# Performance work log

Measured on AMD Instinct MI355X. Metric: run time of the kernel, lower is better.

## Reference

```python
import jax, jax.numpy as jnp
import numpy as np

B, L, D, H = 4, 2048, 1024, 64  # batch, seq, d_model, head_size

def setup_inputs() -> dict:
    key = jax.random.key(0)
    k1, k2 = jax.random.split(key)
    x = jax.random.normal(k1, (B, L, D), dtype=jnp.float32)
    # nn.Linear(d_model, head_size, bias=False) weight: [head_size, d_model]
    Wq = jax.random.normal(k2, (H, D), dtype=jnp.float32) * (1.0 / np.sqrt(D))
    return {"x": x, "Wq": Wq}

def reference(x, Wq):
    # Faithful to source bug: q, k, v ALL use the query projection.
    q = jnp.einsum('bld,hd->blh', x, Wq)
    k = q
    v = q
    d_k = x.shape[-1]  # source uses d_model, not head_size
    scores = jnp.einsum('blh,bmh->blm', q, k) / jnp.sqrt(jnp.float32(d_k))
    Lq = x.shape[1]
    causal = jnp.tril(jnp.ones((Lq, Lq), dtype=bool))
    scores = jnp.where(causal, scores, -jnp.inf)
    attn = jax.nn.softmax(scores, axis=-1)
    # dropout in eval mode -> identity
    return jnp.einsum('blm,bmh->blh', attn, v)
```

## Files before the change

### kernel.cpp

```cpp
#include <hip/hip_runtime.h>
#include <cmath>

#define Bb 4
#define Ll 2048
#define Dd 1024
#define Hh 64

#define QSCL 0.21233050f

typedef float f32x4 __attribute__((ext_vector_type(4)));
typedef short s16x8 __attribute__((ext_vector_type(8)));

__device__ __forceinline__ unsigned int cvtpk(float a, float b) {
    unsigned int r;
    asm("v_cvt_pk_bf16_f32 %0, %1, %2" : "=v"(r) : "v"(a), "v"(b));
    return r;
}

__device__ __forceinline__ void gload16(const void* g, void* l) {
    __builtin_amdgcn_global_load_lds((__attribute__((address_space(1))) const void*)g,
                                     (__attribute__((address_space(3))) void*)l, 16, 0, 0);
}

__global__ __launch_bounds__(256) void wq_cvt(const float* __restrict__ Wq,
                                              unsigned short* __restrict__ wqb) {
    const int idx = blockIdx.x * 256 + threadIdx.x;
    const int c   = idx >> 11;
    const int kc  = (idx >> 6) & 31;
    const int hsw = idx & 63;
    const int h   = hsw ^ kc;
    const float* src = Wq + (size_t)h * Dd + c * 256 + kc * 8;
    float4 a = *(const float4*)src;
    float4 b = *(const float4*)(src + 4);
    uint4 p; p.x = cvtpk(a.x, a.y); p.y = cvtpk(a.z, a.w);
    p.z = cvtpk(b.x, b.y); p.w = cvtpk(b.z, b.w);
    *(uint4*)(wqb + (size_t)idx * 8) = p;
}

__global__ __launch_bounds__(256, 2) void proj_mfma(const float* __restrict__ x,
                                                    const unsigned short* __restrict__ wqb,
                                                    unsigned short* __restrict__ q,
                                                    unsigned short* __restrict__ qT) {
    __shared__ uint4 xs4[2][32 * 16];
    __shared__ uint4 ws4[2][32 * 64];
    const int t = threadIdx.x;
    const int lane = t & 63, w = t >> 6;
    const int m15 = lane & 15, q_ = lane >> 4;
    const int row0 = blockIdx.x * 16;
    const int kc = t & 31, rr = t >> 5;
    const float* xsrc0 = x + (size_t)(row0 + rr) * Dd + kc * 8;
    const float* xsrc1 = x + (size_t)(row0 + rr + 8) * Dd + kc * 8;

    float4 xa0 = *(const float4*)xsrc0, xb0 = *(const float4*)(xsrc0 + 4);
    float4 xa1 = *(const float4*)xsrc1, xb1 = *(const float4*)(xsrc1 + 4);
#pragma unroll
    for (int j = 0; j < 8; ++j) {
        int off = t + j * 256;
        gload16(wqb + (size_t)off * 8, (char*)ws4[0] + off * 16);
    }
    {
        uint4 p0; p0.x = cvtpk(xa0.x, xa0.y); p0.y = cvtpk(xa0.z, xa0.w);
        p0.z = cvtpk(xb0.x, xb0.y); p0.w = cvtpk(xb0.z, xb0.w);
        xs4[0][kc * 16 + (rr ^ (kc & 15))] = p0;
        uint4 p1; p1.x = cvtpk(xa1.x, xa1.y); p1.y = cvtpk(xa1.z, xa1.w);
        p1.z = cvtpk(xb1.x, xb1.y); p1.w = cvtpk(xb1.z, xb1.w);
        xs4[0][kc * 16 + ((rr + 8) ^ (kc & 15))] = p1;
    }
    xa0 = *(const float4*)(xsrc0 + 256); xb0 = *(const float4*)(xsrc0 + 260);
    xa1 = *(const float4*)(xsrc1 + 256); xb1 = *(const float4*)(xsrc1 + 260);

    f32x4 acc = {0.f, 0.f, 0.f, 0.f};
    for (int c = 0; c < 4; ++c) {
        const int p = c & 1;
        __syncthreads();
        if (c + 1 < 4) {
#pragma unroll
            for (int j = 0; j < 8; ++j) {
                int off = t + j * 256;
                gload16(wqb + (size_t)(c + 1) * 16384 + (size_t)off * 8,
                        (char*)ws4[p ^ 1] + off * 16);
            }
            uint4 p0; p0.x = cvtpk(xa0.x, xa0.y); p0.y = cvtpk(xa0.z, xa0.w);
            p0.z = cvtpk(xb0.x, xb0.y); p0.w = cvtpk(xb0.z, xb0.w);
            xs4[p ^ 1][kc * 16 + (rr ^ (kc & 15))] = p0;
            uint4 p1; p1.x = cvtpk(xa1.x, xa1.y); p1.y = cvtpk(xa1.z, xa1.w);
            p1.z = cvtpk(xb1.x, xb1.y); p1.w = cvtpk(xb1.z, xb1.w);
            xs4[p ^ 1][kc * 16 + ((rr + 8) ^ (kc & 15))] = p1;
            if (c + 2 < 4) {
                xa0 = *(const float4*)(xsrc0 + (c + 2) * 256);
                xb0 = *(const float4*)(xsrc0 + (c + 2) * 256 + 4);
                xa1 = *(const float4*)(xsrc1 + (c + 2) * 256);
                xb1 = *(const float4*)(xsrc1 + (c + 2) * 256 + 4);
            }
        }
#pragma unroll
        for (int ks = 0; ks < 8; ++ks) {
            int kk = ks * 4 + q_;
            s16x8 A = *(const s16x8*)&xs4[p][kk * 16 + (m15 ^ (kk & 15))];
            s16x8 B = *(const s16x8*)&ws4[p][kk * 64 + ((w * 16 + m15) ^ kk)];
            acc = __builtin_amdgcn_mfma_f32_16x16x32_bf16(A, B, acc, 0, 0, 0);
        }
    }
    const int h = w * 16 + m15;
    const int hc = h >> 3, he = h & 7;
    const size_t T = (size_t)(row0 >> 6);
    const int rbase = (row0 & 63) + q_ * 4;
    unsigned int a01 = cvtpk(acc[0] * QSCL, acc[1] * QSCL);
    unsigned int a23 = cvtpk(acc[2] * QSCL, acc[3] * QSCL);
    unsigned short u[4] = { (unsigned short)(a01 & 0xFFFF), (unsigned short)(a01 >> 16),
                            (unsigned short)(a23 & 0xFFFF), (unsigned short)(a23 >> 16) };
#pragma unroll
    for (int i = 0; i < 4; ++i) {
        int rsw = (rbase + i) ^ hc;
        q[((T * 8 + hc) * 64 + rsw) * 8 + he] = u[i];
    }
    unsigned int t01 = cvtpk(acc[0], acc[1]);
    unsigned int t23 = cvtpk(acc[2], acc[3]);
    const int b = row0 >> 11;
    const int m0 = (row0 & 2047) + q_ * 4;
    const int vt = m0 >> 6, cc = (m0 >> 3) & 7, me = m0 & 7;
    const int hsw = h ^ cc;
    ushort4 pk4;
    pk4.x = (unsigned short)(t01 & 0xFFFF); pk4.y = (unsigned short)(t01 >> 16);
    pk4.z = (unsigned short)(t23 & 0xFFFF); pk4.w = (unsigned short)(t23 >> 16);
    *(ushort4*)&qT[(((size_t)(b * 32 + vt) * 8 + cc) * 64 + hsw) * 8 + me] = pk4;
}

__global__ __launch_bounds__(256, 3) void flash_mfma(const unsigned short* __restrict__ qg,
                                                     const unsigned short* __restrict__ qTg,
                                                     float* __restrict__ PO,
                                                     float* __restrict__ ML) {
    const int qt = blockIdx.x;
    const int s  = blockIdx.y;
    const int b  = blockIdx.z;
    if (s > (qt >> 2)) return;
    __shared__ uint4 Qs4[512];
    __shared__ uint4 Ks4[2][512];
    __shared__ uint4 Vt4[2][512];
    __shared__ __align__(16) unsigned short Pb[4 * 16 * 72];
    const int t = threadIdx.x, lane = t & 63, w = t >> 6;
    const int m15 = lane & 15, q_ = lane >> 4;
    const int n_it = min(4, qt - 4 * s + 1);
    const int tb = b * 32;
    const unsigned short* qsrc = qg + (size_t)(tb + qt) * 4096;

#pragma unroll
    for (int j = 0; j < 2; ++j) {
        int off = t + j * 256;
        gload16(qsrc + (size_t)off * 8, (char*)Qs4 + off * 16);
        gload16(qg  + (size_t)(tb + s * 4) * 4096 + (size_t)off * 8, (char*)Ks4[0] + off * 16);
        gload16(qTg + (size_t)(tb + s * 4) * 4096 + (size_t)off * 8, (char*)Vt4[0] + off * 16);
    }
    f32x4 Oacc[4];
#pragma unroll
    for (int i = 0; i < 4; ++i) Oacc[i] = (f32x4){0.f, 0.f, 0.f, 0.f};
    float mr = -INFINITY, lr = 0.f;
    unsigned short* Pr = Pb + (w * 16 + m15) * 72;

    for (int it = 0; it < n_it; ++it) {
        const int pp = it & 1;
        __syncthreads();
        if (it + 1 < n_it) {
            const unsigned short* k2 = qg  + (size_t)(tb + s * 4 + it + 1) * 4096;
            const unsigned short* v2 = qTg + (size_t)(tb + s * 4 + it + 1) * 4096;
#pragma unroll
            for (int j = 0; j < 2; ++j) {
                int off = t + j * 256;
                gload16(k2 + (size_t)off * 8, (char*)Ks4[pp ^ 1] + off * 16);
                gload16(v2 + (size_t)off * 8, (char*)Vt4[pp ^ 1] + off * 16);
            }
        }
        f32x4 sc[4];
#pragma unroll
        for (int ct = 0; ct < 4; ++ct) sc[ct] = (f32x4){0.f, 0.f, 0.f, 0.f};
        __builtin_amdgcn_s_setprio(1);
#pragma unroll
        for (int ks = 0; ks < 2; ++ks) {
            const int hc = ks * 4 + q_;
            s16x8 Bq = *(const s16x8*)&Qs4[hc * 64 + ((w * 16 + m15) ^ hc)];
#pragma unroll
            for (int ct = 0; ct < 4; ++ct) {
                s16x8 Ak = *(const s16x8*)&Ks4[pp][hc * 64 + ((ct * 16 + m15) ^ hc)];
                sc[ct] = __builtin_amdgcn_mfma_f32_16x16x32_bf16(Ak, Bq, sc[ct], 0, 0, 0);
            }
        }
        __builtin_amdgcn_s_setprio(0);

        const bool diag = (4 * s + it) == qt;
        float v[16];
        if (diag) {
            const int rel = w * 16 + m15 - q_ * 4;
#pragma unroll
            for (int ct = 0; ct < 4; ++ct)
#pragma unroll
                for (int r = 0; r < 4; ++r)
                    v[ct * 4 + r] = (ct * 16 + r > rel) ? -INFINITY : sc[ct][r];
        } else {
#pragma unroll
            for (int ct = 0; ct < 4; ++ct)
#pragma unroll
                for (int r = 0; r < 4; ++r)
                    v[ct * 4 + r] = sc[ct][r];
        }
        float x01 = fmaxf(v[0], v[1]),  x23 = fmaxf(v[2], v[3]);
        float x45 = fmaxf(v[4], v[5]),  x67 = fmaxf(v[6], v[7]);
        float x89 = fmaxf(v[8], v[9]),  xab = fmaxf(v[10], v[11]);
        float xcd = fmaxf(v[12], v[13]), xef = fmaxf(v[14], v[15]);
        float vmax = fmaxf(fmaxf(fmaxf(x01, x23), fmaxf(x45, x67)),
                           fmaxf(fmaxf(x89, xab), fmaxf(xcd, xef)));
        vmax = fmaxf(vmax, __shfl_xor(vmax, 16, 64));
        vmax = fmaxf(vmax, __shfl_xor(vmax, 32, 64));
        const float mnew = fmaxf(mr, vmax);
        const float alpha = exp2f(mr - mnew);
#pragma unroll
        for (int i = 0; i < 16; ++i) v[i] = exp2f(v[i] - mnew);
        float s01 = (v[0] + v[1]) + (v[2] + v[3]);
        float s23 = (v[4] + v[5]) + (v[6] + v[7]);
        float s45 = (v[8] + v[9]) + (v[10] + v[11]);
        float s67 = (v[12] + v[13]) + (v[14] + v[15]);
        float psum = (s01 + s23) + (s45 + s67);
        psum += __shfl_xor(psum, 16, 64);
        psum += __shfl_xor(psum, 32, 64);
        lr = lr * alpha + psum;
        mr = mnew;
#pragma unroll
        for (int ht = 0; ht < 4; ++ht) Oacc[ht] *= alpha;
#pragma unroll
        for (int ct = 0; ct < 4; ++ct) {
            uint2 pr; pr.x = cvtpk(v[ct * 4 + 0], v[ct * 4 + 1]);
            pr.y = cvtpk(v[ct * 4 + 2], v[ct * 4 + 3]);
            *(uint2*)(Pr + ct * 16 + q_ * 4) = pr;
        }
        __builtin_amdgcn_s_setprio(1);
#pragma unroll
        for (int kc2 = 0; kc2 < 2; ++kc2) {
            const int cc = kc2 * 4 + q_;
            s16x8 Bp = *(const s16x8*)(Pr + kc2 * 32 + q_ * 8);
#pragma unroll
            for (int ht = 0; ht < 4; ++ht) {
                s16x8 Av = *(const s16x8*)&Vt4[pp][cc * 64 + ((ht * 16 + m15) ^ cc)];
                Oacc[ht] = __builtin_amdgcn_mfma_f32_16x16x32_bf16(Av, Bp, Oacc[ht], 0, 0, 0);
            }
        }
        __builtin_amdgcn_s_setprio(0);
    }
    const size_t base = ((size_t)((b * 32 + qt) * 8 + s)) * 4096;
#pragma unroll
    for (int ht = 0; ht < 4; ++ht)
        *(f32x4*)&PO[base + (size_t)(w * 16 + m15) * 64 + ht * 16 + q_ * 4] = Oacc[ht];
    if (q_ == 0) {
        float* mlp = ML + ((size_t)((b * 32 + qt) * 8 + s)) * 128;
        mlp[(w * 16 + m15) * 2 + 0] = mr;
        mlp[(w * 16 + m15) * 2 + 1] = lr;
    }
}

__global__ __launch_bounds__(256) void combine_k(const float* __restrict__ PO,
                                                 const float* __restrict__ ML,
                                                 float* __restrict__ out) {
    const int bq = blockIdx.x;
    const int b = bq >> 5, qt = bq & 31;
    const int ns = (qt >> 2) + 1;
    const int t = threadIdx.x;
    const int r = blockIdx.y * 32 + (t >> 3);
    const int c8 = (t & 7) * 8;
    const float* mlp = ML + (size_t)bq * 8 * 128;
    const float* pob = PO + (size_t)bq * 8 * 4096;
    float M = -INFINITY;
    for (int si = 0; si < ns; ++si) M = fmaxf(M, mlp[si * 128 + r * 2]);
    float L = 0.f;
    f32x4 a0 = {0.f, 0.f, 0.f, 0.f}, a1 = a0;
    for (int si = 0; si < ns; ++si) {
        float ms = mlp[si * 128 + r * 2], ls = mlp[si * 128 + r * 2 + 1];
        float wgt = exp2f(ms - M);
        L += ls * wgt;
        const f32x4* sp = (const f32x4*)(pob + (size_t)si * 4096 + r * 64 + c8);
        a0 += wgt * sp[0];
        a1 += wgt * sp[1];
    }
    float inv = 1.0f / L;
    f32x4* op = (f32x4*)(out + (size_t)(b * Ll + qt * 64 + r) * 64 + c8);
    op[0] = a0 * inv;
    op[1] = a1 * inv;
}

extern "C" void kernel_launch(void* const* d_in, const int* in_sizes, int n_in,
                              void* d_out, int out_size, void* d_ws, size_t ws_size,
                              hipStream_t stream) {
    const float* x  = (const float*)d_in[0];
    const float* Wq = (const float*)d_in[1];
    float* out = (float*)d_out;
    char* ws = (char*)d_ws;
    unsigned short* q   = (unsigned short*)ws;
    unsigned short* qT  = (unsigned short*)(ws + (1 << 20));
    float* PO = (float*)(ws + (2 << 20));
    float* ML = (float*)(ws + (18 << 20));
    unsigned short* wqb = (unsigned short*)(ws + (19 << 20));

    wq_cvt<<<32, 256, 0, stream>>>(Wq, wqb);
    proj_mfma<<<512, 256, 0, stream>>>(x, wqb, q, qT);
    flash_mfma<<<dim3(32, 8, Bb), 256, 0, stream>>>(q, qT, PO, ML);
    combine_k<<<dim3(128, 2), 256, 0, stream>>>(PO, ML, out);
}
```

Baseline: 103.0 us.

## Fuse split-KV combine into flash kernel via last-block atomic counter, compact grid

Removes the separate combine kernel launch: each flash block bumps a per-query-tile atomic counter after writing its partial output, and the last split block to finish performs the log-sum-exp merge and writes the final output. The grid is also compacted from a 3D grid with early-exit blocks into a triangular 1D enumeration of only the valid (query tile, split) pairs. Counters are zeroed inside the projection kernel. This saves one launch and the idle blocks, at the cost of threadfences and a serialized tail combine on the last-arriving block.

```diff
diff --git a/kernel.cpp b/kernel.cpp
--- a/kernel.cpp
+++ b/kernel.cpp
@@ -40,10 +40,12 @@
 __global__ __launch_bounds__(256, 2) void proj_mfma(const float* __restrict__ x,
                                                     const unsigned short* __restrict__ wqb,
                                                     unsigned short* __restrict__ q,
-                                                    unsigned short* __restrict__ qT) {
+                                                    unsigned short* __restrict__ qT,
+                                                    int* __restrict__ cnt) {
     __shared__ uint4 xs4[2][32 * 16];
     __shared__ uint4 ws4[2][32 * 64];
     const int t = threadIdx.x;
+    if (blockIdx.x == 0 && t < 128) cnt[t] = 0;
     const int lane = t & 63, w = t >> 6;
     const int m15 = lane & 15, q_ = lane >> 4;
     const int row0 = blockIdx.x * 16;
@@ -129,15 +131,23 @@
 __global__ __launch_bounds__(256, 3) void flash_mfma(const unsigned short* __restrict__ qg,
                                                      const unsigned short* __restrict__ qTg,
                                                      float* __restrict__ PO,
-                                                     float* __restrict__ ML) {
-    const int qt = blockIdx.x;
-    const int s  = blockIdx.y;
-    const int b  = blockIdx.z;
-    if (s > (qt >> 2)) return;
+                                                     float* __restrict__ ML,
+                                                     int* __restrict__ cnt,
+                                                     float* __restrict__ out) {
+    const int idx = blockIdx.x;
+    const int b   = blockIdx.y;
+    int g = 0;
+    while (2 * (g + 1) * (g + 2) <= idx) ++g;
+    const int local = idx - 2 * g * (g + 1);
+    const int qt = 4 * g + local / (g + 1);
+    const int s  = local % (g + 1);
+    const int ns = g + 1;
+
     __shared__ uint4 Qs4[512];
     __shared__ uint4 Ks4[2][512];
     __shared__ uint4 Vt4[2][512];
     __shared__ __align__(16) unsigned short Pb[4 * 16 * 72];
+    __shared__ int lastFlag;
     const int t = threadIdx.x, lane = t & 63, w = t >> 6;
     const int m15 = lane & 15, q_ = lane >> 4;
     const int n_it = min(4, qt - 4 * s + 1);
@@ -244,44 +254,48 @@
         }
         __builtin_amdgcn_s_setprio(0);
     }
-    const size_t base = ((size_t)((b * 32 + qt) * 8 + s)) * 4096;
+    const int bq = b * 32 + qt;
+    const size_t base = ((size_t)bq * 8 + s) * 4096;
 #pragma unroll
     for (int ht = 0; ht < 4; ++ht)
         *(f32x4*)&PO[base + (size_t)(w * 16 + m15) * 64 + ht * 16 + q_ * 4] = Oacc[ht];
     if (q_ == 0) {
-        float* mlp = ML + ((size_t)((b * 32 + qt) * 8 + s)) * 128;
+        float* mlp = ML + ((size_t)bq * 8 + s) * 128;
         mlp[(w * 16 + m15) * 2 + 0] = mr;
         mlp[(w * 16 + m15) * 2 + 1] = lr;
     }
-}
-
-__global__ __launch_bounds__(256) void combine_k(const float* __restrict__ PO,
-                                                 const float* __restrict__ ML,
-                                                 float* __restrict__ out) {
-    const int bq = blockIdx.x;
-    const int b = bq >> 5, qt = bq & 31;
-    const int ns = (qt >> 2) + 1;
-    const int t = threadIdx.x;
-    const int r = blockIdx.y * 32 + (t >> 3);
-    const int c8 = (t & 7) * 8;
+    __threadfence();
+    __syncthreads();
+    if (t == 0) {
+        int old = atomicAdd(&cnt[bq], 1);
+        lastFlag = (old == ns - 1);
+    }
+    __syncthreads();
+    if (!lastFlag) return;
+    __threadfence();
     const float* mlp = ML + (size_t)bq * 8 * 128;
     const float* pob = PO + (size_t)bq * 8 * 4096;
-    float M = -INFINITY;
-    for (int si = 0; si < ns; ++si) M = fmaxf(M, mlp[si * 128 + r * 2]);
-    float L = 0.f;
-    f32x4 a0 = {0.f, 0.f, 0.f, 0.f}, a1 = a0;
-    for (int si = 0; si < ns; ++si) {
-        float ms = mlp[si * 128 + r * 2], ls = mlp[si * 128 + r * 2 + 1];
-        float wgt = exp2f(ms - M);
-        L += ls * wgt;
-        const f32x4* sp = (const f32x4*)(pob + (size_t)si * 4096 + r * 64 + c8);
-        a0 += wgt * sp[0];
-        a1 += wgt * sp[1];
-    }
-    float inv = 1.0f / L;
-    f32x4* op = (f32x4*)(out + (size_t)(b * Ll + qt * 64 + r) * 64 + c8);
-    op[0] = a0 * inv;
-    op[1] = a1 * inv;
+    const int c8 = (t & 7) * 8;
+#pragma unroll
+    for (int ry = 0; ry < 2; ++ry) {
+        const int r = ry * 32 + (t >> 3);
+        float M = -INFINITY;
+        for (int si = 0; si < ns; ++si) M = fmaxf(M, mlp[si * 128 + r * 2]);
+        float L = 0.f;
+        f32x4 a0 = {0.f, 0.f, 0.f, 0.f}, a1 = a0;
+        for (int si = 0; si < ns; ++si) {
+            float ms = mlp[si * 128 + r * 2], ls = mlp[si * 128 + r * 2 + 1];
+            float wgt = exp2f(ms - M);
+            L += ls * wgt;
+            const f32x4* sp = (const f32x4*)(pob + (size_t)si * 4096 + r * 64 + c8);
+            a0 += wgt * sp[0];
+            a1 += wgt * sp[1];
+        }
+        float inv = 1.0f / L;
+        f32x4* op = (f32x4*)(out + (size_t)(b * Ll + qt * 64 + r) * 64 + c8);
+        op[0] = a0 * inv;
+        op[1] = a1 * inv;
+    }
 }
 
 extern "C" void kernel_launch(void* const* d_in, const int* in_sizes, int n_in,
@@ -296,9 +310,9 @@
     float* PO = (float*)(ws + (2 << 20));
     float* ML = (float*)(ws + (18 << 20));
     unsigned short* wqb = (unsigned short*)(ws + (19 << 20));
+    int* cnt = (int*)(ws + (20 << 20));
 
     wq_cvt<<<32, 256, 0, stream>>>(Wq, wqb);
-    proj_mfma<<<512, 256, 0, stream>>>(x, wqb, q, qT);
-    flash_mfma<<<dim3(32, 8, Bb), 256, 0, stream>>>(q, qT, PO, ML);
-    combine_k<<<dim3(128, 2), 256, 0, stream>>>(PO, ML, out);
-}
+    proj_mfma<<<512, 256, 0, stream>>>(x, wqb, q, qT, cnt);
+    flash_mfma<<<dim3(144, Bb), 256, 0, stream>>>(q, qT, PO, ML, cnt, out);
+}
```

After: 188.9 us. +83.4%, slower.

## Drop split-KV partitioning and normalize attention output directly in flash kernel

Applied to the files above, without the earlier changes.

Each flash block now walks every causal key tile for its query tile instead of at most four. It divides by the running softmax sum and writes the final output itself. This removes the partial-output and max/sum workspace writes and the separate combine kernel launch. The cost is a grid of only 128 blocks with very uneven work: the last query tile runs 32 iterations serially, which can leave many CUs idle and lengthen the critical path.

```diff
diff --git a/kernel.cpp b/kernel.cpp
--- a/kernel.cpp
+++ b/kernel.cpp
@@ -128,19 +128,16 @@
 
 __global__ __launch_bounds__(256, 3) void flash_mfma(const unsigned short* __restrict__ qg,
                                                      const unsigned short* __restrict__ qTg,
-                                                     float* __restrict__ PO,
-                                                     float* __restrict__ ML) {
+                                                     float* __restrict__ out) {
     const int qt = blockIdx.x;
-    const int s  = blockIdx.y;
-    const int b  = blockIdx.z;
-    if (s > (qt >> 2)) return;
+    const int b  = blockIdx.y;
     __shared__ uint4 Qs4[512];
     __shared__ uint4 Ks4[2][512];
     __shared__ uint4 Vt4[2][512];
     __shared__ __align__(16) unsigned short Pb[4 * 16 * 72];
     const int t = threadIdx.x, lane = t & 63, w = t >> 6;
     const int m15 = lane & 15, q_ = lane >> 4;
-    const int n_it = min(4, qt - 4 * s + 1);
+    const int n_it = qt + 1;
     const int tb = b * 32;
     const unsigned short* qsrc = qg + (size_t)(tb + qt) * 4096;
 
@@ -148,8 +145,8 @@
     for (int j = 0; j < 2; ++j) {
         int off = t + j * 256;
         gload16(qsrc + (size_t)off * 8, (char*)Qs4 + off * 16);
-        gload16(qg  + (size_t)(tb + s * 4) * 4096 + (size_t)off * 8, (char*)Ks4[0] + off * 16);
-        gload16(qTg + (size_t)(tb + s * 4) * 4096 + (size_t)off * 8, (char*)Vt4[0] + off * 16);
+        gload16(qg  + (size_t)tb * 4096 + (size_t)off * 8, (char*)Ks4[0] + off * 16);
+        gload16(qTg + (size_t)tb * 4096 + (size_t)off * 8, (char*)Vt4[0] + off * 16);
     }
     f32x4 Oacc[4];
 #pragma unroll
@@ -161,8 +158,8 @@
         const int pp = it & 1;
         __syncthreads();
         if (it + 1 < n_it) {
-            const unsigned short* k2 = qg  + (size_t)(tb + s * 4 + it + 1) * 4096;
-            const unsigned short* v2 = qTg + (size_t)(tb + s * 4 + it + 1) * 4096;
+            const unsigned short* k2 = qg  + (size_t)(tb + it + 1) * 4096;
+            const unsigned short* v2 = qTg + (size_t)(tb + it + 1) * 4096;
 #pragma unroll
             for (int j = 0; j < 2; ++j) {
                 int off = t + j * 256;
@@ -186,7 +183,7 @@
         }
         __builtin_amdgcn_s_setprio(0);
 
-        const bool diag = (4 * s + it) == qt;
+        const bool diag = (it == qt);
         float v[16];
         if (diag) {
             const int rel = w * 16 + m15 - q_ * 4;
@@ -244,44 +241,13 @@
         }
         __builtin_amdgcn_s_setprio(0);
     }
-    const size_t base = ((size_t)((b * 32 + qt) * 8 + s)) * 4096;
-#pragma unroll
-    for (int ht = 0; ht < 4; ++ht)
-        *(f32x4*)&PO[base + (size_t)(w * 16 + m15) * 64 + ht * 16 + q_ * 4] = Oacc[ht];
-    if (q_ == 0) {
-        float* mlp = ML + ((size_t)((b * 32 + qt) * 8 + s)) * 128;
-        mlp[(w * 16 + m15) * 2 + 0] = mr;
-        mlp[(w * 16 + m15) * 2 + 1] = lr;
-    }
-}
-
-__global__ __launch_bounds__(256) void combine_k(const float* __restrict__ PO,
-                                                 const float* __restrict__ ML,
-                                                 float* __restrict__ out) {
-    const int bq = blockIdx.x;
-    const int b = bq >> 5, qt = bq & 31;
-    const int ns = (qt >> 2) + 1;
-    const int t = threadIdx.x;
-    const int r = blockIdx.y * 32 + (t >> 3);
-    const int c8 = (t & 7) * 8;
-    const float* mlp = ML + (size_t)bq * 8 * 128;
-    const float* pob = PO + (size_t)bq * 8 * 4096;
-    float M = -INFINITY;
-    for (int si = 0; si < ns; ++si) M = fmaxf(M, mlp[si * 128 + r * 2]);
-    float L = 0.f;
-    f32x4 a0 = {0.f, 0.f, 0.f, 0.f}, a1 = a0;
-    for (int si = 0; si < ns; ++si) {
-        float ms = mlp[si * 128 + r * 2], ls = mlp[si * 128 + r * 2 + 1];
-        float wgt = exp2f(ms - M);
-        L += ls * wgt;
-        const f32x4* sp = (const f32x4*)(pob + (size_t)si * 4096 + r * 64 + c8);
-        a0 += wgt * sp[0];
-        a1 += wgt * sp[1];
-    }
-    float inv = 1.0f / L;
-    f32x4* op = (f32x4*)(out + (size_t)(b * Ll + qt * 64 + r) * 64 + c8);
-    op[0] = a0 * inv;
-    op[1] = a1 * inv;
+    const float inv = 1.0f / lr;
+    const size_t obase = (size_t)(b * Ll + qt * 64 + w * 16 + m15) * 64;
+#pragma unroll
+    for (int ht = 0; ht < 4; ++ht) {
+        f32x4 o = Oacc[ht] * inv;
+        *(f32x4*)&out[obase + ht * 16 + q_ * 4] = o;
+    }
 }
 
 extern "C" void kernel_launch(void* const* d_in, const int* in_sizes, int n_in,
@@ -293,12 +259,9 @@
     char* ws = (char*)d_ws;
     unsigned short* q   = (unsigned short*)ws;
     unsigned short* qT  = (unsigned short*)(ws + (1 << 20));
-    float* PO = (float*)(ws + (2 << 20));
-    float* ML = (float*)(ws + (18 << 20));
-    unsigned short* wqb = (unsigned short*)(ws + (19 << 20));
+    unsigned short* wqb = (unsigned short*)(ws + (2 << 20));
 
     wq_cvt<<<32, 256, 0, stream>>>(Wq, wqb);
     proj_mfma<<<512, 256, 0, stream>>>(x, wqb, q, qT);
-    flash_mfma<<<dim3(32, 8, Bb), 256, 0, stream>>>(q, qT, PO, ML);
-    combine_k<<<dim3(128, 2), 256, 0, stream>>>(PO, ML, out);
-}
+    flash_mfma<<<dim3(32, Bb), 256, 0, stream>>>(q, qT, out);
+}
```

Result: slower. 122.7 us (+19.2%).

## Fuse Wq bf16 conversion into projection and compact flash grid to valid blocks

Applied to the files above, without the earlier changes.

Removes the separate Wq conversion kernel: each projection block now loads fp32 Wq rows directly, converts to bf16 and writes the swizzled layout into LDS itself. This drops one launch and the intermediate buffer, but every one of the 512 blocks redoes the conversion with synchronous loads instead of async global-to-LDS copies. The flash kernel grid is compacted from 32x8xB, with most blocks exiting early, to 144xB blocks that map a linear index to the valid (qt, split) pairs through a small loop. This avoids launching and scheduling empty blocks.

```diff
diff --git a/kernel.cpp b/kernel.cpp
--- a/kernel.cpp
+++ b/kernel.cpp
@@ -22,23 +22,8 @@
                                      (__attribute__((address_space(3))) void*)l, 16, 0, 0);
 }
 
-__global__ __launch_bounds__(256) void wq_cvt(const float* __restrict__ Wq,
-                                              unsigned short* __restrict__ wqb) {
-    const int idx = blockIdx.x * 256 + threadIdx.x;
-    const int c   = idx >> 11;
-    const int kc  = (idx >> 6) & 31;
-    const int hsw = idx & 63;
-    const int h   = hsw ^ kc;
-    const float* src = Wq + (size_t)h * Dd + c * 256 + kc * 8;
-    float4 a = *(const float4*)src;
-    float4 b = *(const float4*)(src + 4);
-    uint4 p; p.x = cvtpk(a.x, a.y); p.y = cvtpk(a.z, a.w);
-    p.z = cvtpk(b.x, b.y); p.w = cvtpk(b.z, b.w);
-    *(uint4*)(wqb + (size_t)idx * 8) = p;
-}
-
 __global__ __launch_bounds__(256, 2) void proj_mfma(const float* __restrict__ x,
-                                                    const unsigned short* __restrict__ wqb,
+                                                    const float* __restrict__ Wq,
                                                     unsigned short* __restrict__ q,
                                                     unsigned short* __restrict__ qT) {
     __shared__ uint4 xs4[2][32 * 16];
@@ -55,8 +40,14 @@
     float4 xa1 = *(const float4*)xsrc1, xb1 = *(const float4*)(xsrc1 + 4);
 #pragma unroll
     for (int j = 0; j < 8; ++j) {
-        int off = t + j * 256;
-        gload16(wqb + (size_t)off * 8, (char*)ws4[0] + off * 16);
+        int idx2 = t + j * 256;
+        int kcw = idx2 & 31, hw = (idx2 >> 5) & 63;
+        const float* wsrc = Wq + (size_t)hw * Dd + kcw * 8;
+        float4 a = *(const float4*)wsrc;
+        float4 b2 = *(const float4*)(wsrc + 4);
+        uint4 p; p.x = cvtpk(a.x, a.y); p.y = cvtpk(a.z, a.w);
+        p.z = cvtpk(b2.x, b2.y); p.w = cvtpk(b2.z, b2.w);
+        ws4[0][kcw * 64 + (hw ^ kcw)] = p;
     }
     {
         uint4 p0; p0.x = cvtpk(xa0.x, xa0.y); p0.y = cvtpk(xa0.z, xa0.w);
@@ -74,11 +65,17 @@
         const int p = c & 1;
         __syncthreads();
         if (c + 1 < 4) {
+            const int k0n = (c + 1) * 256;
 #pragma unroll
             for (int j = 0; j < 8; ++j) {
-                int off = t + j * 256;
-                gload16(wqb + (size_t)(c + 1) * 16384 + (size_t)off * 8,
-                        (char*)ws4[p ^ 1] + off * 16);
+                int idx2 = t + j * 256;
+                int kcw = idx2 & 31, hw = (idx2 >> 5) & 63;
+                const float* wsrc = Wq + (size_t)hw * Dd + k0n + kcw * 8;
+                float4 a = *(const float4*)wsrc;
+                float4 b2 = *(const float4*)(wsrc + 4);
+                uint4 pw; pw.x = cvtpk(a.x, a.y); pw.y = cvtpk(a.z, a.w);
+                pw.z = cvtpk(b2.x, b2.y); pw.w = cvtpk(b2.z, b2.w);
+                ws4[p ^ 1][kcw * 64 + (hw ^ kcw)] = pw;
             }
             uint4 p0; p0.x = cvtpk(xa0.x, xa0.y); p0.y = cvtpk(xa0.z, xa0.w);
             p0.z = cvtpk(xb0.x, xb0.y); p0.w = cvtpk(xb0.z, xb0.w);
@@ -130,10 +127,14 @@
                                                      const unsigned short* __restrict__ qTg,
                                                      float* __restrict__ PO,
                                                      float* __restrict__ ML) {
-    const int qt = blockIdx.x;
-    const int s  = blockIdx.y;
-    const int b  = blockIdx.z;
-    if (s > (qt >> 2)) return;
+    const int idx = blockIdx.x;
+    const int b   = blockIdx.y;
+    int g = 0;
+    while (2 * (g + 1) * (g + 2) <= idx) ++g;
+    const int local = idx - 2 * g * (g + 1);
+    const int qt = 4 * g + local / (g + 1);
+    const int s  = local % (g + 1);
+
     __shared__ uint4 Qs4[512];
     __shared__ uint4 Ks4[2][512];
     __shared__ uint4 Vt4[2][512];
@@ -244,12 +245,13 @@
         }
         __builtin_amdgcn_s_setprio(0);
     }
-    const size_t base = ((size_t)((b * 32 + qt) * 8 + s)) * 4096;
+    const int bq = b * 32 + qt;
+    const size_t base = ((size_t)bq * 8 + s) * 4096;
 #pragma unroll
     for (int ht = 0; ht < 4; ++ht)
         *(f32x4*)&PO[base + (size_t)(w * 16 + m15) * 64 + ht * 16 + q_ * 4] = Oacc[ht];
     if (q_ == 0) {
-        float* mlp = ML + ((size_t)((b * 32 + qt) * 8 + s)) * 128;
+        float* mlp = ML + ((size_t)bq * 8 + s) * 128;
         mlp[(w * 16 + m15) * 2 + 0] = mr;
         mlp[(w * 16 + m15) * 2 + 1] = lr;
     }
@@ -295,10 +297,8 @@
     unsigned short* qT  = (unsigned short*)(ws + (1 << 20));
     float* PO = (float*)(ws + (2 << 20));
     float* ML = (float*)(ws + (18 << 20));
-    unsigned short* wqb = (unsigned short*)(ws + (19 << 20));
-
-    wq_cvt<<<32, 256, 0, stream>>>(Wq, wqb);
-    proj_mfma<<<512, 256, 0, stream>>>(x, wqb, q, qT);
-    flash_mfma<<<dim3(32, 8, Bb), 256, 0, stream>>>(q, qT, PO, ML);
+
+    proj_mfma<<<512, 256, 0, stream>>>(x, Wq, q, qT);
+    flash_mfma<<<dim3(144, Bb), 256, 0, stream>>>(q, qT, PO, ML);
     combine_k<<<dim3(128, 2), 256, 0, stream>>>(PO, ML, out);
 }
```

New measurement: 99.97 us. -2.9%, faster.
